# Performance work log

Hardware: AMD Instinct MI355X
Metric: run time of the kernel (lower is better)

Reference implementation:

```python
import jax, jax.numpy as jnp
import numpy as np

F = 64        # atom feature dim (from Linear(64, 32))
N_RBF = 25    # Gaussian RBF expansion size (standard SchNet 0..5 A)
CUTOFF = 5.0
GAMMA = 10.0  # RBF width parameter: exp(-gamma * (d - mu)^2)


def ssp(x):
    # shifted softplus: ln(0.5 * e^x + 0.5) = softplus(x) - ln 2
    return jax.nn.softplus(x) - jnp.log(2.0).astype(x.dtype)


def setup_inputs() -> dict:
    key = jax.random.key(0)
    ks = jax.random.split(key, 16)
    B, N = 4, 512
    embedding = jax.random.normal(ks[0], (B, N, F), jnp.float32)
    d = jax.random.uniform(ks[1], (B, N, N), jnp.float32) * CUTOFF
    distances = 0.5 * (d + jnp.swapaxes(d, 1, 2))  # symmetric pairwise distances
    s = 0.1
    # 3 stacked interaction blocks
    in2f = jax.random.normal(ks[2], (3, F, F), jnp.float32) * s      # atomwise in->filter (no bias)
    fw1 = jax.random.normal(ks[3], (3, N_RBF, F), jnp.float32) * s   # filter net layer 1
    fb1 = jnp.zeros((3, F), jnp.float32)
    fw2 = jax.random.normal(ks[4], (3, F, F), jnp.float32) * s       # filter net layer 2
    fb2 = jnp.zeros((3, F), jnp.float32)
    f2o = jax.random.normal(ks[5], (3, F, F), jnp.float32) * s       # filter->out atomwise
    f2b = jnp.zeros((3, F), jnp.float32)
    dw = jax.random.normal(ks[6], (3, F, F), jnp.float32) * s        # output atomwise
    db = jnp.zeros((3, F), jnp.float32)
    # readout MLP: Linear(64,32) + SSP + Linear(32,1)
    aw1 = jax.random.normal(ks[7], (F, 32), jnp.float32) * s
    ab1 = jnp.zeros((32,), jnp.float32)
    aw2 = jax.random.normal(ks[8], (32, 1), jnp.float32) * s
    ab2 = jnp.zeros((1,), jnp.float32)
    return dict(embedding=embedding, distances=distances, in2f=in2f, fw1=fw1,
                fb1=fb1, fw2=fw2, fb2=fb2, f2o=f2o, f2b=f2b, dw=dw, db=db,
                aw1=aw1, ab1=ab1, aw2=aw2, ab2=ab2)


def reference(embedding, distances, in2f, fw1, fb1, fw2, fb2, f2o, f2b, dw, db,
              aw1, ab1, aw2, ab2):
    dtype = embedding.dtype
    centers = jnp.linspace(0.0, CUTOFF, N_RBF).astype(dtype)
    # Gaussian RBF expansion of pairwise distances: [B, N, N, N_RBF]
    rbf = jnp.exp(-GAMMA * jnp.square(distances[..., None] - centers))
    x = embedding  # [B, N, F]
    for i in range(3):
        f = x @ in2f[i]  # [B, N, F]
        # filter-generating network on expanded distances -> [B, N, N, F]
        W = ssp(jnp.einsum('bijr,rf->bijf', rbf, fw1[i]) + fb1[i])
        W = W @ fw2[i] + fb2[i]
        # continuous-filter convolution: y_i = sum_j f_j * W_ij
        y = jnp.einsum('bjf,bijf->bif', f, W)
        y = ssp(y @ f2o[i] + f2b[i])
        y = y @ dw[i] + db[i]
        x = x + y  # residual
    h = ssp(x @ aw1 + ab1)   # [B, N, 32]
    return h @ aw2 + ab2     # [B, N, 1]
```

## Files before the change

### kernel.cpp

```cpp
#include <hip/hip_runtime.h>

#define KBIN 224
#define TSTRIDE 68
#define TPSZ  15232
#define FBASE 15232

typedef _Float16 half2v __attribute__((ext_vector_type(2)));

__device__ __forceinline__ float ssp(float x) {
    return fmaxf(x, 0.0f) + log1pf(expf(-fabsf(x))) - 0.69314718055994531f;
}

__device__ __forceinline__ float bclane(float v, int l) {
    return __builtin_bit_cast(float, __builtin_amdgcn_readlane(__builtin_bit_cast(int, v), l));
}

__device__ __forceinline__ float matvec64(const float* __restrict__ ldsA, int base, float xv, int lane) {
    float a0 = 0.f, a1 = 0.f, a2 = 0.f, a3 = 0.f;
    #pragma unroll
    for (int gg = 0; gg < 16; ++gg) {
        const float4 w = *(const float4*)&ldsA[base + lane*64 + (((gg + lane) & 15) << 2)];
        a0 += bclane(xv, gg*4+0) * w.x;
        a1 += bclane(xv, gg*4+1) * w.y;
        a2 += bclane(xv, gg*4+2) * w.z;
        a3 += bclane(xv, gg*4+3) * w.w;
    }
    return (a0 + a1) + (a2 + a3);
}

__device__ __forceinline__ void matvec64x2(const float* __restrict__ ldsA, int base,
                                           float xv0, float xv1, int lane,
                                           float& o0, float& o1) {
    float a0 = 0.f, a1 = 0.f, b0 = 0.f, b1 = 0.f;
    #pragma unroll
    for (int gg = 0; gg < 16; ++gg) {
        const float4 w = *(const float4*)&ldsA[base + lane*64 + (((gg + lane) & 15) << 2)];
        a0 += bclane(xv0, gg*4+0) * w.x;
        a1 += bclane(xv0, gg*4+1) * w.y;
        a0 += bclane(xv0, gg*4+2) * w.z;
        a1 += bclane(xv0, gg*4+3) * w.w;
        b0 += bclane(xv1, gg*4+0) * w.x;
        b1 += bclane(xv1, gg*4+1) * w.y;
        b0 += bclane(xv1, gg*4+2) * w.z;
        b1 += bclane(xv1, gg*4+3) * w.w;
    }
    o0 = a0 + a1;
    o1 = b0 + b1;
}

__device__ __forceinline__ void stageWT(float* __restrict__ lds, int base, const float* __restrict__ W, int tid) {
    for (int s = tid; s < 4096; s += 512) {
        int f = s >> 6, g = s & 63;
        lds[base + g*64 + ((((f >> 2) + g) & 15) << 2) + (f & 3)] = W[s];
    }
}

__global__ __launch_bounds__(512) void schnet_pre0(
    const float* __restrict__ emb,
    const float* __restrict__ in2f,
    const float* __restrict__ fw1, const float* __restrict__ fb1,
    const float* __restrict__ fw2, const float* __restrict__ fb2,
    unsigned short* __restrict__ f_out, unsigned int* __restrict__ Tp_g)
{
    __shared__ float lds[12544];
    const int wg = blockIdx.x, tid = threadIdx.x;
    const int wave = tid >> 6, lane = tid & 63;
    if (wg < 128) {
        stageWT(lds, 0, in2f, tid);
        __syncthreads();
        int row0 = wg*16 + wave*2;
        size_t ro0 = (size_t)row0*64 + lane;
        size_t ro1 = ro0 + 64;
        float f0, f1;
        matvec64x2(lds, 0, emb[ro0], emb[ro1], lane, f0, f1);
        f_out[ro0] = __builtin_bit_cast(unsigned short, (_Float16)f0);
        f_out[ro1] = __builtin_bit_cast(unsigned short, (_Float16)f1);
    } else {
        int widx = wg - 128;
        int tt = widx / 28;
        int k = (widx % 28)*8 + wave;
        const float* fw1t = fw1 + tt*25*64;
        const float* fw2t = fw2 + tt*64*64;
        for (int s = tid; s < 1600; s += 512) lds[s] = fw1t[s];
        for (int s = tid; s < 4096; s += 512) lds[1600 + s] = fw2t[s];
        if (tid < 64) { lds[5696 + tid] = fb1[tt*64 + tid]; lds[5760 + tid] = fb2[tt*64 + tid]; }
        __syncthreads();
        float T2[2];
        #pragma unroll
        for (int e = 0; e < 2; ++e) {
            float dk = (float)(k + e) * (5.0f/224.0f);
            float h1 = lds[5696 + lane];
            for (int r = 0; r < 25; ++r) {
                float sr = dk - (float)r * (5.0f/24.0f);
                h1 += expf(-10.0f*sr*sr) * lds[r*64 + lane];
            }
            float u = ssp(h1);
            float T = lds[5760 + lane];
            #pragma unroll
            for (int gg = 0; gg < 64; ++gg)
                T += bclane(u, gg) * lds[1600 + gg*64 + lane];
            T2[e] = T;
        }
        float* sc = &lds[5824 + wave*128];
        sc[lane] = T2[0];
        sc[64 + lane] = T2[1];
        if (lane < 16) {
            float4 A  = *(const float4*)&sc[lane*4];
            float4 Bv = *(const float4*)&sc[64 + lane*4];
            half2v t01 = { (_Float16)A.x, (_Float16)A.y };
            half2v t23 = { (_Float16)A.z, (_Float16)A.w };
            half2v d01 = { (_Float16)(Bv.x - A.x), (_Float16)(Bv.y - A.y) };
            half2v d23 = { (_Float16)(Bv.z - A.z), (_Float16)(Bv.w - A.w) };
            uint4 o;
            o.x = __builtin_bit_cast(unsigned int, t01);
            o.y = __builtin_bit_cast(unsigned int, t23);
            o.z = __builtin_bit_cast(unsigned int, d01);
            o.w = __builtin_bit_cast(unsigned int, d23);
            *(uint4*)&Tp_g[(size_t)tt*TPSZ + k*TSTRIDE + lane*4] = o;
        }
    }
}

__global__ __launch_bounds__(512, 4) void schnet_block(
    int t,
    const float* __restrict__ emb, const float* __restrict__ dists,
    const float* __restrict__ in2f,
    const float* __restrict__ f2o, const float* __restrict__ f2b,
    const float* __restrict__ dw,  const float* __restrict__ db,
    const float* __restrict__ aw1, const float* __restrict__ ab1,
    const float* __restrict__ aw2, const float* __restrict__ ab2,
    const unsigned int* __restrict__ Tp_g,
    const unsigned short* __restrict__ f_in,
    unsigned short* __restrict__ f_out,
    float* __restrict__ x_buf, float* __restrict__ out)
{
    __shared__ unsigned int ldsu[FBASE + 4096];
    float* lds = (float*)ldsu;
    const int wg = blockIdx.x, tid = threadIdx.x;
    const int wave = tid >> 6, lane = tid & 63;
    const int b = wg >> 7, it = wg & 127;
    const int i0 = it * 4;
    const int fq = lane & 15, g = lane >> 4;
    const int r = wave >> 1;
    const int jhalf = wave & 1;

    const unsigned int* Tp = Tp_g + (size_t)t*TPSZ;
    for (int s = tid; s < TPSZ/4; s += 512)
        ((uint4*)ldsu)[s] = ((const uint4*)Tp)[s];

    const unsigned int* Tbase = ldsu + fq*4;
    const unsigned int* ftb = ldsu + FBASE + fq*256;
    const float scale = 224.0f/5.0f;
    float a0 = 0.f, a1 = 0.f, a2 = 0.f, a3 = 0.f;

    for (int c = 0; c < 4; ++c) {
        if (c) __syncthreads();
        for (int s = tid; s < 2048; s += 512) {
            int j = s >> 4, fqq = s & 15;
            const unsigned int* src = (const unsigned int*)&f_in[((size_t)b*512 + c*128 + j)*64 + fqq*4];
            int jp = j >> 1;
            unsigned int* dst = &ldsu[FBASE + fqq*256 + (((jp + fqq) & 63) << 2) + (j & 1)*2];
            dst[0] = src[0]; dst[1] = src[1];
        }
        __syncthreads();
        const float4* dp = (const float4*)&dists[((size_t)(b*512 + i0 + r))*512 + c*128 + jhalf*64 + g*16];
        float4 dq[4];
        #pragma unroll
        for (int q = 0; q < 4; ++q) dq[q] = dp[q];
        const int jp_base = jhalf*32 + g*8;
        #pragma unroll
        for (int j4 = 0; j4 < 4; ++j4) {
            uint4 fA = *(const uint4*)&ftb[((jp_base + j4*2 + fq) & 63) << 2];
            uint4 fB = *(const uint4*)&ftb[((jp_base + j4*2 + 1 + fq) & 63) << 2];
            float dd[4] = {dq[j4].x, dq[j4].y, dq[j4].z, dq[j4].w};
            unsigned int fl_[8] = {fA.x, fA.y, fA.z, fA.w, fB.x, fB.y, fB.z, fB.w};
            #pragma unroll
            for (int u = 0; u < 4; ++u) {
                float tv = fminf(fmaxf(dd[u], 0.0f)*scale, 223.999f);
                int k = (int)tv;
                float fr = tv - (float)k;
                uint4 tp = *(const uint4*)&Tbase[k*TSTRIDE];
                _Float16 ah = (_Float16)fr;
                half2v av = { ah, ah };
                half2v W01 = __builtin_bit_cast(half2v, tp.z)*av + __builtin_bit_cast(half2v, tp.x);
                half2v W23 = __builtin_bit_cast(half2v, tp.w)*av + __builtin_bit_cast(half2v, tp.y);
                half2v f01 = __builtin_bit_cast(half2v, fl_[u*2]);
                half2v f23 = __builtin_bit_cast(half2v, fl_[u*2+1]);
                a0 += (float)W01[0] * (float)f01[0];
                a1 += (float)W01[1] * (float)f01[1];
                a2 += (float)W23[0] * (float)f23[0];
                a3 += (float)W23[1] * (float)f23[1];
            }
        }
    }
    a0 += __shfl_xor(a0, 16, 64); a0 += __shfl_xor(a0, 32, 64);
    a1 += __shfl_xor(a1, 16, 64); a1 += __shfl_xor(a1, 32, 64);
    a2 += __shfl_xor(a2, 16, 64); a2 += __shfl_xor(a2, 32, 64);
    a3 += __shfl_xor(a3, 16, 64); a3 += __shfl_xor(a3, 32, 64);

    __syncthreads();
    if (g == 0) {
        float4 acc; acc.x = a0; acc.y = a1; acc.z = a2; acc.w = a3;
        *(float4*)&lds[FBASE + wave*64 + fq*4] = acc;
    }
    stageWT(lds, 0, f2o + t*4096, tid);
    stageWT(lds, 4096, dw + t*4096, tid);
    if (t < 2) {
        stageWT(lds, 8192, in2f + (t+1)*4096, tid);
    } else {
        for (int s = tid; s < 4096; s += 512) {
            int f = s >> 6, rr = s & 63;
            lds[8192 + rr*64 + ((((f >> 2) + rr) & 15) << 2) + (f & 3)] = aw1[f*32 + (rr & 31)];
        }
    }
    if (tid < 64) {
        lds[12288 + tid] = f2b[t*64 + tid];
        lds[12352 + tid] = db[t*64 + tid];
        if (t == 2) {
            lds[12416 + tid] = ab1[tid & 31];
            lds[12480 + tid] = aw2[tid & 31];
        }
    }
    __syncthreads();

    if (wave < 4) {
        int grow = b*512 + i0 + wave;
        size_t ro = (size_t)grow*64 + lane;
        float y = lds[FBASE + (wave*2)*64 + lane] + lds[FBASE + (wave*2+1)*64 + lane];
        float z = matvec64(lds, 0, y, lane) + lds[12288 + lane];
        float u = ssp(z);
        float y3 = matvec64(lds, 4096, u, lane) + lds[12352 + lane];
        float xin = (t == 0) ? emb[ro] : x_buf[ro];
        float xn = xin + y3;
        if (t < 2) {
            x_buf[ro] = xn;
            float fo = matvec64(lds, 8192, xn, lane);
            f_out[ro] = __builtin_bit_cast(unsigned short, (_Float16)fo);
        } else {
            float s1 = matvec64(lds, 8192, xn, lane) + lds[12416 + lane];
            float h = ssp(s1) * lds[12480 + lane];
            #pragma unroll
            for (int m = 1; m < 64; m <<= 1)
                h += __shfl_xor(h, m, 64);
            if (lane == 0) out[grow] = ab2[0] + 0.5f*h;
        }
    }
}

extern "C" void kernel_launch(void* const* d_in, const int* in_sizes, int n_in,
                              void* d_out, int out_size, void* d_ws, size_t ws_size,
                              hipStream_t stream) {
    const float* emb  = (const float*)d_in[0];
    const float* dist = (const float*)d_in[1];
    const float* in2f = (const float*)d_in[2];
    const float* fw1  = (const float*)d_in[3];
    const float* fb1  = (const float*)d_in[4];
    const float* fw2  = (const float*)d_in[5];
    const float* fb2  = (const float*)d_in[6];
    const float* f2o  = (const float*)d_in[7];
    const float* f2b  = (const float*)d_in[8];
    const float* dwp  = (const float*)d_in[9];
    const float* dbp  = (const float*)d_in[10];
    const float* aw1  = (const float*)d_in[11];
    const float* ab1  = (const float*)d_in[12];
    const float* aw2  = (const float*)d_in[13];
    const float* ab2  = (const float*)d_in[14];
    float* out = (float*)d_out;
    float* ws = (float*)d_ws;
    unsigned int* Tp_g = (unsigned int*)ws;
    unsigned short* fA = (unsigned short*)(ws + 45696);
    unsigned short* fB = (unsigned short*)(ws + 45696 + 65536);
    float* x_buf = ws + 45696 + 2*65536;

    hipLaunchKernelGGL(schnet_pre0, dim3(212), dim3(512), 0, stream,
        emb, in2f, fw1, fb1, fw2, fb2, fA, Tp_g);
    hipLaunchKernelGGL(schnet_block, dim3(512), dim3(512), 0, stream,
        0, emb, dist, in2f, f2o, f2b, dwp, dbp, aw1, ab1, aw2, ab2,
        Tp_g, fA, fB, x_buf, out);
    hipLaunchKernelGGL(schnet_block, dim3(512), dim3(512), 0, stream,
        1, emb, dist, in2f, f2o, f2b, dwp, dbp, aw1, ab1, aw2, ab2,
        Tp_g, fB, fA, x_buf, out);
    hipLaunchKernelGGL(schnet_block, dim3(512), dim3(512), 0, stream,
        2, emb, dist, in2f, f2o, f2b, dwp, dbp, aw1, ab1, aw2, ab2,
        Tp_g, fA, fB, x_buf, out);
}
```

Baseline: 75.04 us.

## Precompute packed distance-bin indices once and software-pipeline feature staging

Adds 256 blocks to the pre-kernel that convert each distance once into a packed word holding a byte offset into the filter table and an fp16 fraction. The three interaction blocks then read these words instead of recomputing the bin from fp32 distances, and use a byte permute to splat the fraction. The feature-tile staging in the block kernel is restructured: the next chunk is loaded into registers while the current chunk is computed, and the swizzled layout is replaced with a plain one. This trades extra pre-kernel work and a 4 MB workspace buffer for less per-pair ALU work and hidden global latency, at the risk of LDS bank conflicts from dropping the swizzle.

```diff
diff --git a/kernel.cpp b/kernel.cpp
--- a/kernel.cpp
+++ b/kernel.cpp
@@ -13,6 +13,14 @@
 
 __device__ __forceinline__ float bclane(float v, int l) {
     return __builtin_bit_cast(float, __builtin_amdgcn_readlane(__builtin_bit_cast(int, v), l));
+}
+
+__device__ __forceinline__ unsigned int kaenc(float d) {
+    float tv = fminf(fmaxf(d, 0.0f)*(224.0f/5.0f), 223.999f);
+    int k = (int)tv;
+    float fr = tv - (float)k;
+    unsigned short fh = __builtin_bit_cast(unsigned short, (_Float16)fr);
+    return ((unsigned int)(k*272) << 16) | (unsigned int)fh;
 }
 
 __device__ __forceinline__ float matvec64(const float* __restrict__ ldsA, int base, float xv, int lane) {
@@ -56,11 +64,12 @@
 }
 
 __global__ __launch_bounds__(512) void schnet_pre0(
-    const float* __restrict__ emb,
+    const float* __restrict__ emb, const float* __restrict__ dists,
     const float* __restrict__ in2f,
     const float* __restrict__ fw1, const float* __restrict__ fb1,
     const float* __restrict__ fw2, const float* __restrict__ fb2,
-    unsigned short* __restrict__ f_out, unsigned int* __restrict__ Tp_g)
+    unsigned short* __restrict__ f_out, unsigned int* __restrict__ Tp_g,
+    unsigned int* __restrict__ ka)
 {
     __shared__ float lds[12544];
     const int wg = blockIdx.x, tid = threadIdx.x;
@@ -75,7 +84,7 @@
         matvec64x2(lds, 0, emb[ro0], emb[ro1], lane, f0, f1);
         f_out[ro0] = __builtin_bit_cast(unsigned short, (_Float16)f0);
         f_out[ro1] = __builtin_bit_cast(unsigned short, (_Float16)f1);
-    } else {
+    } else if (wg < 212) {
         int widx = wg - 128;
         int tt = widx / 28;
         int k = (widx % 28)*8 + wave;
@@ -118,18 +127,28 @@
             o.w = __builtin_bit_cast(unsigned int, d23);
             *(uint4*)&Tp_g[(size_t)tt*TPSZ + k*TSTRIDE + lane*4] = o;
         }
+    } else {
+        size_t p = (size_t)(wg - 212)*4096 + (size_t)tid*8;
+        float4 d0 = *(const float4*)&dists[p];
+        float4 d1 = *(const float4*)&dists[p + 4];
+        uint4 o0, o1;
+        o0.x = kaenc(d0.x); o0.y = kaenc(d0.y); o0.z = kaenc(d0.z); o0.w = kaenc(d0.w);
+        o1.x = kaenc(d1.x); o1.y = kaenc(d1.y); o1.z = kaenc(d1.z); o1.w = kaenc(d1.w);
+        *(uint4*)&ka[p] = o0;
+        *(uint4*)&ka[p + 4] = o1;
     }
 }
 
 __global__ __launch_bounds__(512, 4) void schnet_block(
     int t,
-    const float* __restrict__ emb, const float* __restrict__ dists,
+    const float* __restrict__ emb,
     const float* __restrict__ in2f,
     const float* __restrict__ f2o, const float* __restrict__ f2b,
     const float* __restrict__ dw,  const float* __restrict__ db,
     const float* __restrict__ aw1, const float* __restrict__ ab1,
     const float* __restrict__ aw2, const float* __restrict__ ab2,
     const unsigned int* __restrict__ Tp_g,
+    const unsigned int* __restrict__ ka,
     const unsigned short* __restrict__ f_in,
     unsigned short* __restrict__ f_out,
     float* __restrict__ x_buf, float* __restrict__ out)
@@ -148,40 +167,46 @@
     for (int s = tid; s < TPSZ/4; s += 512)
         ((uint4*)ldsu)[s] = ((const uint4*)Tp)[s];
 
-    const unsigned int* Tbase = ldsu + fq*4;
-    const unsigned int* ftb = ldsu + FBASE + fq*256;
-    const float scale = 224.0f/5.0f;
+    const int j0 = tid >> 4, fq2 = tid & 15;
+    const uint2* fsrc0 = (const uint2*)f_in + ((size_t)b*512 + j0)*16 + fq2;
+    unsigned int* fdst = ldsu + FBASE + (j0 >> 1)*64 + fq2*4 + (j0 & 1)*2;
+    uint2 rb0, rb1, rb2, rb3;
+    {
+        const uint2* sp = fsrc0;
+        rb0 = sp[0]; rb1 = sp[512]; rb2 = sp[1024]; rb3 = sp[1536];
+        *(uint2*)fdst = rb0; *(uint2*)(fdst + 1024) = rb1;
+        *(uint2*)(fdst + 2048) = rb2; *(uint2*)(fdst + 3072) = rb3;
+    }
+    __syncthreads();
+
+    const unsigned int* kabase = &ka[((size_t)(b*512 + i0 + r))*512 + jhalf*64 + g*16];
+    const unsigned int* fp = ldsu + FBASE + fq*4;
+    const char* Tbyte = (const char*)ldsu + fq*16;
+    const int jpb = jhalf*32 + g*8;
     float a0 = 0.f, a1 = 0.f, a2 = 0.f, a3 = 0.f;
 
     for (int c = 0; c < 4; ++c) {
-        if (c) __syncthreads();
-        for (int s = tid; s < 2048; s += 512) {
-            int j = s >> 4, fqq = s & 15;
-            const unsigned int* src = (const unsigned int*)&f_in[((size_t)b*512 + c*128 + j)*64 + fqq*4];
-            int jp = j >> 1;
-            unsigned int* dst = &ldsu[FBASE + fqq*256 + (((jp + fqq) & 63) << 2) + (j & 1)*2];
-            dst[0] = src[0]; dst[1] = src[1];
-        }
-        __syncthreads();
-        const float4* dp = (const float4*)&dists[((size_t)(b*512 + i0 + r))*512 + c*128 + jhalf*64 + g*16];
-        float4 dq[4];
-        #pragma unroll
-        for (int q = 0; q < 4; ++q) dq[q] = dp[q];
-        const int jp_base = jhalf*32 + g*8;
+        if (c < 3) {
+            const uint2* sp = fsrc0 + (size_t)(c + 1)*2048;
+            rb0 = sp[0]; rb1 = sp[512]; rb2 = sp[1024]; rb3 = sp[1536];
+        }
+        uint4 kq0 = ((const uint4*)(kabase + c*128))[0];
+        uint4 kq1 = ((const uint4*)(kabase + c*128))[1];
+        uint4 kq2 = ((const uint4*)(kabase + c*128))[2];
+        uint4 kq3 = ((const uint4*)(kabase + c*128))[3];
+        uint4 kqa[4] = {kq0, kq1, kq2, kq3};
         #pragma unroll
         for (int j4 = 0; j4 < 4; ++j4) {
-            uint4 fA = *(const uint4*)&ftb[((jp_base + j4*2 + fq) & 63) << 2];
-            uint4 fB = *(const uint4*)&ftb[((jp_base + j4*2 + 1 + fq) & 63) << 2];
-            float dd[4] = {dq[j4].x, dq[j4].y, dq[j4].z, dq[j4].w};
+            uint4 fA = *(const uint4*)&fp[(jpb + j4*2)*64];
+            uint4 fB = *(const uint4*)&fp[(jpb + j4*2 + 1)*64];
+            unsigned int kk[4] = {kqa[j4].x, kqa[j4].y, kqa[j4].z, kqa[j4].w};
             unsigned int fl_[8] = {fA.x, fA.y, fA.z, fA.w, fB.x, fB.y, fB.z, fB.w};
             #pragma unroll
             for (int u = 0; u < 4; ++u) {
-                float tv = fminf(fmaxf(dd[u], 0.0f)*scale, 223.999f);
-                int k = (int)tv;
-                float fr = tv - (float)k;
-                uint4 tp = *(const uint4*)&Tbase[k*TSTRIDE];
-                _Float16 ah = (_Float16)fr;
-                half2v av = { ah, ah };
+                unsigned int kau = kk[u];
+                unsigned int koff = kau >> 16;
+                half2v av = __builtin_bit_cast(half2v, __builtin_amdgcn_perm(kau, kau, 0x01000100u));
+                uint4 tp = *(const uint4*)(Tbyte + koff);
                 half2v W01 = __builtin_bit_cast(half2v, tp.z)*av + __builtin_bit_cast(half2v, tp.x);
                 half2v W23 = __builtin_bit_cast(half2v, tp.w)*av + __builtin_bit_cast(half2v, tp.y);
                 half2v f01 = __builtin_bit_cast(half2v, fl_[u*2]);
@@ -191,6 +216,12 @@
                 a2 += (float)W23[0] * (float)f23[0];
                 a3 += (float)W23[1] * (float)f23[1];
             }
+        }
+        if (c < 3) {
+            __syncthreads();
+            *(uint2*)fdst = rb0; *(uint2*)(fdst + 1024) = rb1;
+            *(uint2*)(fdst + 2048) = rb2; *(uint2*)(fdst + 3072) = rb3;
+            __syncthreads();
         }
     }
     a0 += __shfl_xor(a0, 16, 64); a0 += __shfl_xor(a0, 32, 64);
@@ -271,16 +302,17 @@
     unsigned short* fA = (unsigned short*)(ws + 45696);
     unsigned short* fB = (unsigned short*)(ws + 45696 + 65536);
     float* x_buf = ws + 45696 + 2*65536;
-
-    hipLaunchKernelGGL(schnet_pre0, dim3(212), dim3(512), 0, stream,
-        emb, in2f, fw1, fb1, fw2, fb2, fA, Tp_g);
+    unsigned int* ka = (unsigned int*)(x_buf + 131072);
+
+    hipLaunchKernelGGL(schnet_pre0, dim3(468), dim3(512), 0, stream,
+        emb, dist, in2f, fw1, fb1, fw2, fb2, fA, Tp_g, ka);
     hipLaunchKernelGGL(schnet_block, dim3(512), dim3(512), 0, stream,
-        0, emb, dist, in2f, f2o, f2b, dwp, dbp, aw1, ab1, aw2, ab2,
-        Tp_g, fA, fB, x_buf, out);
+        0, emb, in2f, f2o, f2b, dwp, dbp, aw1, ab1, aw2, ab2,
+        Tp_g, ka, fA, fB, x_buf, out);
     hipLaunchKernelGGL(schnet_block, dim3(512), dim3(512), 0, stream,
-        1, emb, dist, in2f, f2o, f2b, dwp, dbp, aw1, ab1, aw2, ab2,
-        Tp_g, fB, fA, x_buf, out);
+        1, emb, in2f, f2o, f2b, dwp, dbp, aw1, ab1, aw2, ab2,
+        Tp_g, ka, fB, fA, x_buf, out);
     hipLaunchKernelGGL(schnet_block, dim3(512), dim3(512), 0, stream,
-        2, emb, dist, in2f, f2o, f2b, dwp, dbp, aw1, ab1, aw2, ab2,
-        Tp_g, fA, fB, x_buf, out);
-}
+        2, emb, in2f, f2o, f2b, dwp, dbp, aw1, ab1, aw2, ab2,
+        Tp_g, ka, fA, fB, x_buf, out);
+}
```

New measurement: 64.56 us. 14.0% less time.
